# Optimization experiments

Measured on AMD Instinct MI355X. Metric: run time of the kernel, lower is better.

## Reference

```python
import jax, jax.numpy as jnp
import numpy as np

B, N, IN_F, OUT_F, H = 16, 1024, 256, 256, 4
D = OUT_F // H  # head_dim = 64
NEG_SLOPE = 0.2


def setup_inputs() -> dict:
    key = jax.random.key(0)
    k1, k2, k3 = jax.random.split(key, 3)
    h = jax.random.normal(k1, (B, N, IN_F), dtype=jnp.float32)
    mask = jnp.ones((B, N), dtype=jnp.int32)
    W = jax.random.normal(k2, (OUT_F, IN_F), dtype=jnp.float32) * (1.0 / np.sqrt(IN_F))
    a = jax.random.normal(k3, (2 * D, 1), dtype=jnp.float32) * 0.1
    return {"h": h, "mask": mask, "W": W, "a": a}


def reference(h, mask, W, a):
    # Wh = h @ W.T -> (B, N, OUT_F) -> (B, H, N, D)
    Wh = jnp.einsum('bnf,of->bno', h, W)
    Wh = Wh.reshape(h.shape[0], h.shape[1], H, D).transpose(0, 2, 1, 3)
    # Additive split: cat([Wh_i, Wh_j]) @ a == Wh_i @ a1 + Wh_j @ a2 (same math,
    # avoids the O(N^2 * 2D) concat tensor)
    a1 = a[:D, 0]  # (D,)
    a2 = a[D:, 0]  # (D,)
    s1 = jnp.einsum('bhnd,d->bhn', Wh, a1)  # score for node i
    s2 = jnp.einsum('bhnd,d->bhn', Wh, a2)  # score for node j
    e = s1[:, :, :, None] + s2[:, :, None, :]          # (B, H, N, N)
    e = jnp.where(e >= 0, e, NEG_SLOPE * e)            # LeakyReLU(0.2)
    node_mask = mask.astype(bool)                      # (B, N)
    mm = node_mask[:, None, :, None] & node_mask[:, None, None, :]  # (B,1,N,N)
    e = jnp.where(mm, e, -jnp.inf)
    attn = jax.nn.softmax(e, axis=-1)
    # dropout is identity in eval mode
    attn = jnp.where(mm, attn, 0.0)
    h_prime = jnp.einsum('bhij,bhjd->bhid', attn, Wh)  # (B, H, N, D)
    h_prime = h_prime.transpose(0, 2, 1, 3).reshape(h.shape[0], h.shape[1], OUT_F)
    return h_prime * mask.astype(h_prime.dtype)[:, :, None]
```

## Files before the change

kernel.cpp:

```cpp
#include <hip/hip_runtime.h>

typedef short short8 __attribute__((ext_vector_type(8)));
typedef float floatx4 __attribute__((ext_vector_type(4)));

#define NEG_SLOPE 0.2f

__device__ __forceinline__ unsigned short f2b(float x) {
    unsigned u = __float_as_uint(x);
    u += 0x7fffu + ((u >> 16) & 1u);
    return (unsigned short)(u >> 16);
}
__device__ __forceinline__ float b2f(unsigned short s) {
    return __uint_as_float(((unsigned)s) << 16);
}
__device__ __forceinline__ void cvt4(float4 v, ushort4& hi, ushort4& lo) {
    hi.x = f2b(v.x); hi.y = f2b(v.y); hi.z = f2b(v.z); hi.w = f2b(v.w);
    lo.x = f2b(v.x - b2f(hi.x)); lo.y = f2b(v.y - b2f(hi.y));
    lo.z = f2b(v.z - b2f(hi.z)); lo.w = f2b(v.w - b2f(hi.w));
}

__global__ __launch_bounds__(256) void k_wh(
    const float* __restrict__ hin, const int* __restrict__ mask,
    const float* __restrict__ W, const float* __restrict__ a,
    unsigned short* __restrict__ WhbT, float2* __restrict__ E1F1,
    float2* __restrict__ E2F2)
{
    __shared__ unsigned short Ahi[64 * 72], Alo[64 * 72];
    __shared__ unsigned short Bhi[128 * 72], Blo[128 * 72];

    const int t = threadIdx.x;
    const int bi = blockIdx.x;
    const int mb = bi & 15, cb = (bi >> 4) & 1, b = bi >> 5;
    const int m0 = mb * 64, n0 = cb * 128;
    const int wid = t >> 6, lane = t & 63;
    const int wm = wid >> 1, wn = wid & 1;
    const int l15 = lane & 15, q = lane >> 4;

    floatx4 acc[2][4];
#pragma unroll
    for (int mt = 0; mt < 2; ++mt)
#pragma unroll
        for (int nt = 0; nt < 4; ++nt) {
            floatx4 z = {0.f, 0.f, 0.f, 0.f};
            acc[mt][nt] = z;
        }

    for (int kt = 0; kt < 4; ++kt) {
        const int k0 = kt * 64;
#pragma unroll
        for (int p = 0; p < 4; ++p) {
            int idx = t + 256 * p;
            int row = idx >> 4, c4 = idx & 15;
            float4 v = *(const float4*)&hin[((size_t)(b * 1024 + m0 + row)) * 256 + k0 + c4 * 4];
            ushort4 hi, lo;
            cvt4(v, hi, lo);
            *(ushort4*)&Ahi[row * 72 + c4 * 4] = hi;
            *(ushort4*)&Alo[row * 72 + c4 * 4] = lo;
        }
#pragma unroll
        for (int p = 0; p < 8; ++p) {
            int idx = t + 256 * p;
            int row = idx >> 4, c4 = idx & 15;
            float4 v = *(const float4*)&W[((size_t)(n0 + row)) * 256 + k0 + c4 * 4];
            ushort4 hi, lo;
            cvt4(v, hi, lo);
            *(ushort4*)&Bhi[row * 72 + c4 * 4] = hi;
            *(ushort4*)&Blo[row * 72 + c4 * 4] = lo;
        }
        __syncthreads();
#pragma unroll
        for (int ks = 0; ks < 2; ++ks) {
            short8 ah[2], al[2], bh[4], bl[4];
#pragma unroll
            for (int mt = 0; mt < 2; ++mt) {
                int r = wm * 32 + mt * 16 + l15;
                ah[mt] = *(const short8*)&Ahi[r * 72 + ks * 32 + q * 8];
                al[mt] = *(const short8*)&Alo[r * 72 + ks * 32 + q * 8];
            }
#pragma unroll
            for (int nt = 0; nt < 4; ++nt) {
                int r = wn * 64 + nt * 16 + l15;
                bh[nt] = *(const short8*)&Bhi[r * 72 + ks * 32 + q * 8];
                bl[nt] = *(const short8*)&Blo[r * 72 + ks * 32 + q * 8];
            }
#pragma unroll
            for (int mt = 0; mt < 2; ++mt)
#pragma unroll
                for (int nt = 0; nt < 4; ++nt) {
                    acc[mt][nt] = __builtin_amdgcn_mfma_f32_16x16x32_bf16(ah[mt], bh[nt], acc[mt][nt], 0, 0, 0);
                    acc[mt][nt] = __builtin_amdgcn_mfma_f32_16x16x32_bf16(ah[mt], bl[nt], acc[mt][nt], 0, 0, 0);
                    acc[mt][nt] = __builtin_amdgcn_mfma_f32_16x16x32_bf16(al[mt], bh[nt], acc[mt][nt], 0, 0, 0);
                }
        }
        __syncthreads();
    }

    const int hh = cb * 2 + wn;
    const int b4h = b * 4 + hh;

    float a1v[4], a2v[4];
#pragma unroll
    for (int nt = 0; nt < 4; ++nt) {
        a1v[nt] = a[nt * 16 + l15];
        a2v[nt] = a[64 + nt * 16 + l15];
    }

#pragma unroll
    for (int mt = 0; mt < 2; ++mt)
#pragma unroll
        for (int nt = 0; nt < 4; ++nt) {
            int d = nt * 16 + l15;
            int i0r = m0 + wm * 32 + mt * 16 + q * 4;
            ushort4 wv;
            wv.x = f2b(acc[mt][nt][0]);
            wv.y = f2b(acc[mt][nt][1]);
            wv.z = f2b(acc[mt][nt][2]);
            wv.w = f2b(acc[mt][nt][3]);
            *(ushort4*)&WhbT[((size_t)(b4h * 64 + d)) * 1024 + i0r] = wv;
        }

    float s1p[2][4], s2p[2][4];
#pragma unroll
    for (int mt = 0; mt < 2; ++mt)
#pragma unroll
        for (int r = 0; r < 4; ++r) {
            float s1 = 0.f, s2 = 0.f;
#pragma unroll
            for (int nt = 0; nt < 4; ++nt) {
                s1 += acc[mt][nt][r] * a1v[nt];
                s2 += acc[mt][nt][r] * a2v[nt];
            }
            s1p[mt][r] = s1;
            s2p[mt][r] = s2;
        }
#pragma unroll
    for (int off = 1; off <= 8; off <<= 1)
#pragma unroll
        for (int mt = 0; mt < 2; ++mt)
#pragma unroll
            for (int r = 0; r < 4; ++r) {
                s1p[mt][r] += __shfl_xor(s1p[mt][r], off, 64);
                s2p[mt][r] += __shfl_xor(s2p[mt][r], off, 64);
            }

    if (l15 == 0) {
#pragma unroll
        for (int mt = 0; mt < 2; ++mt)
#pragma unroll
            for (int r = 0; r < 4; ++r) {
                int i = m0 + wm * 32 + mt * 16 + q * 4 + r;
                float s1 = s1p[mt][r], s2 = s2p[mt][r];
                E1F1[(size_t)b4h * 1024 + i] = make_float2(__expf(s1), __expf(NEG_SLOPE * s1));
                int mj = mask[b * 1024 + i];
                float e2 = mj ? __expf(s2) : 0.f;
                float g2 = mj ? __expf(NEG_SLOPE * s2) : 0.f;
                E2F2[(size_t)b4h * 1024 + i] = make_float2(e2, g2);
            }
    }
}

__global__ __launch_bounds__(256) void k_attn(
    const int* __restrict__ mask,
    const unsigned short* __restrict__ WhbT,
    const float2* __restrict__ E1F1, const float2* __restrict__ E2F2,
    float* __restrict__ out)
{
    __shared__ unsigned short sB[64 * 136];
    __shared__ float2 sEF[128];

    const int t = threadIdx.x;
    const int bi = blockIdx.x;
    const int ib = bi & 7, hh = (bi >> 3) & 3, b = bi >> 5;
    const int i0 = ib * 128;
    const int b4h = b * 4 + hh;
    const int wid = t >> 6, lane = t & 63;
    const int l15 = lane & 15, q = lane >> 4;
    const int iw = i0 + wid * 32;

    float E1v[2], F1v[2];
#pragma unroll
    for (int mt = 0; mt < 2; ++mt) {
        float2 e = E1F1[(size_t)b4h * 1024 + iw + mt * 16 + l15];
        E1v[mt] = e.x;
        F1v[mt] = e.y;
    }

    floatx4 acc[2][4];
#pragma unroll
    for (int mt = 0; mt < 2; ++mt)
#pragma unroll
        for (int nt = 0; nt < 4; ++nt) {
            floatx4 z = {0.f, 0.f, 0.f, 0.f};
            acc[mt][nt] = z;
        }
    float rs[2] = {0.f, 0.f};

    for (int jt = 0; jt < 8; ++jt) {
        const int j0 = jt * 128;
#pragma unroll
        for (int p = 0; p < 4; ++p) {
            int c = t + 256 * p;
            int d = c >> 4, jc = c & 15;
            *(int4*)&sB[d * 136 + jc * 8] =
                *(const int4*)&WhbT[((size_t)(b4h * 64 + d)) * 1024 + j0 + jc * 8];
        }
        if (t < 128) sEF[t] = E2F2[(size_t)b4h * 1024 + j0 + t];
        __syncthreads();

#pragma unroll
        for (int ks = 0; ks < 4; ++ks) {
            const int jl = ks * 32 + q * 8;
            float2 ef[8];
#pragma unroll
            for (int jj = 0; jj < 8; ++jj) ef[jj] = sEF[jl + jj];
            short8 bf[4];
#pragma unroll
            for (int nt = 0; nt < 4; ++nt)
                bf[nt] = *(const short8*)&sB[(nt * 16 + l15) * 136 + jl];
#pragma unroll
            for (int mt = 0; mt < 2; ++mt) {
                short8 af;
                float r0 = 0.f;
#pragma unroll
                for (int jj = 0; jj < 8; ++jj) {
                    float w = fmaxf(E1v[mt] * ef[jj].x, F1v[mt] * ef[jj].y);
                    r0 += w;
                    af[jj] = (short)f2b(w);
                }
                rs[mt] += r0;
#pragma unroll
                for (int nt = 0; nt < 4; ++nt)
                    acc[mt][nt] = __builtin_amdgcn_mfma_f32_16x16x32_bf16(af, bf[nt], acc[mt][nt], 0, 0, 0);
            }
        }
        __syncthreads();
    }

#pragma unroll
    for (int mt = 0; mt < 2; ++mt) {
        rs[mt] += __shfl_xor(rs[mt], 16, 64);
        rs[mt] += __shfl_xor(rs[mt], 32, 64);
    }

#pragma unroll
    for (int mt = 0; mt < 2; ++mt)
#pragma unroll
        for (int r = 0; r < 4; ++r) {
            int i = iw + mt * 16 + q * 4 + r;
            float l = __shfl(rs[mt], q * 4 + r, 64);
            int mi = mask[b * 1024 + i];
            float inv = (mi && l > 0.f) ? 1.0f / l : 0.f;
#pragma unroll
            for (int nt = 0; nt < 4; ++nt)
                out[((size_t)(b * 1024 + i)) * 256 + hh * 64 + nt * 16 + l15] =
                    acc[mt][nt][r] * inv;
        }
}

extern "C" void kernel_launch(void* const* d_in, const int* in_sizes, int n_in,
                              void* d_out, int out_size, void* d_ws, size_t ws_size,
                              hipStream_t stream) {
    const float* h = (const float*)d_in[0];
    const int* mask = (const int*)d_in[1];
    const float* W = (const float*)d_in[2];
    const float* a = (const float*)d_in[3];
    float* out = (float*)d_out;

    unsigned short* WhbT = (unsigned short*)d_ws;
    float2* E1F1 = (float2*)((char*)d_ws + (size_t)16 * 4 * 64 * 1024 * 2);
    float2* E2F2 = E1F1 + 16 * 4 * 1024;

    hipLaunchKernelGGL(k_wh, dim3(512), dim3(256), 0, stream, h, mask, W, a, WhbT, E1F1, E2F2);
    hipLaunchKernelGGL(k_attn, dim3(512), dim3(256), 0, stream, mask, WhbT, E1F1, E2F2, out);
}
```

Before: 108.6 us.

## Store Wh in MFMA fragment layout and double-buffer attention loads via global_load_lds

The projection kernel now writes Wh in the exact per-lane MFMA B-fragment order, and the attention kernel streams it into LDS with direct global-to-LDS loads. It double-buffers those tiles so the next tile loads while the current one computes. Both kernels use smaller tiles and twice as many blocks, with occupancy hints, and head scores are reduced across warps through shared memory. Float-to-bf16 conversion switches to byte-permute packing; the hi/lo split and the attention weights now truncate instead of rounding. This reduces LDS transpose traffic and load latency, at the cost of slightly different rounding in the weights and row sums.

```diff
diff --git a/kernel.cpp b/kernel.cpp
--- a/kernel.cpp
+++ b/kernel.cpp
@@ -2,45 +2,56 @@
 
 typedef short short8 __attribute__((ext_vector_type(8)));
 typedef float floatx4 __attribute__((ext_vector_type(4)));
+typedef unsigned int u32;
 
 #define NEG_SLOPE 0.2f
 
-__device__ __forceinline__ unsigned short f2b(float x) {
-    unsigned u = __float_as_uint(x);
-    u += 0x7fffu + ((u >> 16) & 1u);
-    return (unsigned short)(u >> 16);
-}
-__device__ __forceinline__ float b2f(unsigned short s) {
-    return __uint_as_float(((unsigned)s) << 16);
-}
-__device__ __forceinline__ void cvt4(float4 v, ushort4& hi, ushort4& lo) {
-    hi.x = f2b(v.x); hi.y = f2b(v.y); hi.z = f2b(v.z); hi.w = f2b(v.w);
-    lo.x = f2b(v.x - b2f(hi.x)); lo.y = f2b(v.y - b2f(hi.y));
-    lo.z = f2b(v.z - b2f(hi.z)); lo.w = f2b(v.w - b2f(hi.w));
-}
-
-__global__ __launch_bounds__(256) void k_wh(
+__device__ __forceinline__ u32 pk_rtne(float a, float b) {
+    u32 ua = __float_as_uint(a); ua += 0x7fffu + ((ua >> 16) & 1u);
+    u32 ub = __float_as_uint(b); ub += 0x7fffu + ((ub >> 16) & 1u);
+    return __builtin_amdgcn_perm(ub, ua, 0x07060302);
+}
+__device__ __forceinline__ u32 pk_trunc(float a, float b) {
+    return __builtin_amdgcn_perm(__float_as_uint(b), __float_as_uint(a), 0x07060302);
+}
+__device__ __forceinline__ void split_pk(float a, float b, u32& hi, u32& lo) {
+    u32 ua = __float_as_uint(a), ub = __float_as_uint(b);
+    hi = __builtin_amdgcn_perm(ub, ua, 0x07060302);
+    float la = a - __uint_as_float(ua & 0xffff0000u);
+    float lb = b - __uint_as_float(ub & 0xffff0000u);
+    lo = __builtin_amdgcn_perm(__float_as_uint(lb), __float_as_uint(la), 0x07060302);
+}
+__device__ __forceinline__ void gl_lds16(const void* g, void* l) {
+    __builtin_amdgcn_global_load_lds((__attribute__((address_space(1))) u32*)(void*)g,
+                                     (__attribute__((address_space(3))) u32*)l, 16, 0, 0);
+}
+
+__global__ __launch_bounds__(256, 4) void k_wh(
     const float* __restrict__ hin, const int* __restrict__ mask,
     const float* __restrict__ W, const float* __restrict__ a,
-    unsigned short* __restrict__ WhbT, float2* __restrict__ E1F1,
+    unsigned short* __restrict__ WhF, float2* __restrict__ E1F1,
     float2* __restrict__ E2F2)
 {
     __shared__ unsigned short Ahi[64 * 72], Alo[64 * 72];
-    __shared__ unsigned short Bhi[128 * 72], Blo[128 * 72];
+    __shared__ unsigned short Bhi[64 * 72], Blo[64 * 72];
+    __shared__ float2 sred[2][64];
 
     const int t = threadIdx.x;
     const int bi = blockIdx.x;
-    const int mb = bi & 15, cb = (bi >> 4) & 1, b = bi >> 5;
-    const int m0 = mb * 64, n0 = cb * 128;
+    const int mtile = bi >> 2, cb = bi & 3;
+    const int m0g = mtile * 64;
+    const int b = m0g >> 10;
+    const int i0 = m0g & 1023;
+    const int b4h = b * 4 + cb;
     const int wid = t >> 6, lane = t & 63;
     const int wm = wid >> 1, wn = wid & 1;
     const int l15 = lane & 15, q = lane >> 4;
 
-    floatx4 acc[2][4];
+    floatx4 acc[2][2];
 #pragma unroll
     for (int mt = 0; mt < 2; ++mt)
 #pragma unroll
-        for (int nt = 0; nt < 4; ++nt) {
+        for (int nt = 0; nt < 2; ++nt) {
             floatx4 z = {0.f, 0.f, 0.f, 0.f};
             acc[mt][nt] = z;
         }
@@ -51,26 +62,28 @@
         for (int p = 0; p < 4; ++p) {
             int idx = t + 256 * p;
             int row = idx >> 4, c4 = idx & 15;
-            float4 v = *(const float4*)&hin[((size_t)(b * 1024 + m0 + row)) * 256 + k0 + c4 * 4];
-            ushort4 hi, lo;
-            cvt4(v, hi, lo);
-            *(ushort4*)&Ahi[row * 72 + c4 * 4] = hi;
-            *(ushort4*)&Alo[row * 72 + c4 * 4] = lo;
-        }
-#pragma unroll
-        for (int p = 0; p < 8; ++p) {
+            float4 v = *(const float4*)&hin[((size_t)(m0g + row)) * 256 + k0 + c4 * 4];
+            u32 h0, l0, h1, l1;
+            split_pk(v.x, v.y, h0, l0);
+            split_pk(v.z, v.w, h1, l1);
+            *(uint2*)&Ahi[row * 72 + c4 * 4] = make_uint2(h0, h1);
+            *(uint2*)&Alo[row * 72 + c4 * 4] = make_uint2(l0, l1);
+        }
+#pragma unroll
+        for (int p = 0; p < 4; ++p) {
             int idx = t + 256 * p;
             int row = idx >> 4, c4 = idx & 15;
-            float4 v = *(const float4*)&W[((size_t)(n0 + row)) * 256 + k0 + c4 * 4];
-            ushort4 hi, lo;
-            cvt4(v, hi, lo);
-            *(ushort4*)&Bhi[row * 72 + c4 * 4] = hi;
-            *(ushort4*)&Blo[row * 72 + c4 * 4] = lo;
+            float4 v = *(const float4*)&W[((size_t)(cb * 64 + row)) * 256 + k0 + c4 * 4];
+            u32 h0, l0, h1, l1;
+            split_pk(v.x, v.y, h0, l0);
+            split_pk(v.z, v.w, h1, l1);
+            *(uint2*)&Bhi[row * 72 + c4 * 4] = make_uint2(h0, h1);
+            *(uint2*)&Blo[row * 72 + c4 * 4] = make_uint2(l0, l1);
         }
         __syncthreads();
 #pragma unroll
         for (int ks = 0; ks < 2; ++ks) {
-            short8 ah[2], al[2], bh[4], bl[4];
+            short8 ah[2], al[2], bh[2], bl[2];
 #pragma unroll
             for (int mt = 0; mt < 2; ++mt) {
                 int r = wm * 32 + mt * 16 + l15;
@@ -78,15 +91,15 @@
                 al[mt] = *(const short8*)&Alo[r * 72 + ks * 32 + q * 8];
             }
 #pragma unroll
-            for (int nt = 0; nt < 4; ++nt) {
-                int r = wn * 64 + nt * 16 + l15;
+            for (int nt = 0; nt < 2; ++nt) {
+                int r = wn * 32 + nt * 16 + l15;
                 bh[nt] = *(const short8*)&Bhi[r * 72 + ks * 32 + q * 8];
                 bl[nt] = *(const short8*)&Blo[r * 72 + ks * 32 + q * 8];
             }
 #pragma unroll
             for (int mt = 0; mt < 2; ++mt)
 #pragma unroll
-                for (int nt = 0; nt < 4; ++nt) {
+                for (int nt = 0; nt < 2; ++nt) {
                     acc[mt][nt] = __builtin_amdgcn_mfma_f32_16x16x32_bf16(ah[mt], bh[nt], acc[mt][nt], 0, 0, 0);
                     acc[mt][nt] = __builtin_amdgcn_mfma_f32_16x16x32_bf16(ah[mt], bl[nt], acc[mt][nt], 0, 0, 0);
                     acc[mt][nt] = __builtin_amdgcn_mfma_f32_16x16x32_bf16(al[mt], bh[nt], acc[mt][nt], 0, 0, 0);
@@ -95,43 +108,32 @@
         __syncthreads();
     }
 
-    const int hh = cb * 2 + wn;
-    const int b4h = b * 4 + hh;
-
-    float a1v[4], a2v[4];
-#pragma unroll
-    for (int nt = 0; nt < 4; ++nt) {
-        a1v[nt] = a[nt * 16 + l15];
-        a2v[nt] = a[64 + nt * 16 + l15];
-    }
-
+    const int c32 = (i0 + wm * 32) >> 5;
+#pragma unroll
+    for (int nt = 0; nt < 2; ++nt) {
+        int nt_a = wn * 2 + nt;
+        uint4 v;
+        v.x = pk_rtne(acc[0][nt][0], acc[0][nt][1]);
+        v.y = pk_rtne(acc[0][nt][2], acc[0][nt][3]);
+        v.z = pk_rtne(acc[1][nt][0], acc[1][nt][1]);
+        v.w = pk_rtne(acc[1][nt][2], acc[1][nt][3]);
+        *(uint4*)&WhF[(size_t)(((b4h * 32 + c32) * 4 + nt_a) * 64 + lane) * 8] = v;
+    }
+
+    float a1v[2], a2v[2];
+#pragma unroll
+    for (int nt = 0; nt < 2; ++nt) {
+        int d = wn * 32 + nt * 16 + l15;
+        a1v[nt] = a[d];
+        a2v[nt] = a[64 + d];
+    }
+    float s1p[2][4], s2p[2][4];
 #pragma unroll
     for (int mt = 0; mt < 2; ++mt)
 #pragma unroll
-        for (int nt = 0; nt < 4; ++nt) {
-            int d = nt * 16 + l15;
-            int i0r = m0 + wm * 32 + mt * 16 + q * 4;
-            ushort4 wv;
-            wv.x = f2b(acc[mt][nt][0]);
-            wv.y = f2b(acc[mt][nt][1]);
-            wv.z = f2b(acc[mt][nt][2]);
-            wv.w = f2b(acc[mt][nt][3]);
-            *(ushort4*)&WhbT[((size_t)(b4h * 64 + d)) * 1024 + i0r] = wv;
-        }
-
-    float s1p[2][4], s2p[2][4];
-#pragma unroll
-    for (int mt = 0; mt < 2; ++mt)
-#pragma unroll
         for (int r = 0; r < 4; ++r) {
-            float s1 = 0.f, s2 = 0.f;
-#pragma unroll
-            for (int nt = 0; nt < 4; ++nt) {
-                s1 += acc[mt][nt][r] * a1v[nt];
-                s2 += acc[mt][nt][r] * a2v[nt];
-            }
-            s1p[mt][r] = s1;
-            s2p[mt][r] = s2;
+            s1p[mt][r] = acc[mt][0][r] * a1v[0] + acc[mt][1][r] * a1v[1];
+            s2p[mt][r] = acc[mt][0][r] * a2v[0] + acc[mt][1][r] * a2v[1];
         }
 #pragma unroll
     for (int off = 1; off <= 8; off <<= 1)
@@ -142,119 +144,120 @@
                 s1p[mt][r] += __shfl_xor(s1p[mt][r], off, 64);
                 s2p[mt][r] += __shfl_xor(s2p[mt][r], off, 64);
             }
-
     if (l15 == 0) {
 #pragma unroll
         for (int mt = 0; mt < 2; ++mt)
 #pragma unroll
-            for (int r = 0; r < 4; ++r) {
-                int i = m0 + wm * 32 + mt * 16 + q * 4 + r;
-                float s1 = s1p[mt][r], s2 = s2p[mt][r];
-                E1F1[(size_t)b4h * 1024 + i] = make_float2(__expf(s1), __expf(NEG_SLOPE * s1));
-                int mj = mask[b * 1024 + i];
-                float e2 = mj ? __expf(s2) : 0.f;
-                float g2 = mj ? __expf(NEG_SLOPE * s2) : 0.f;
-                E2F2[(size_t)b4h * 1024 + i] = make_float2(e2, g2);
-            }
-    }
-}
-
-__global__ __launch_bounds__(256) void k_attn(
+            for (int r = 0; r < 4; ++r)
+                sred[wn][wm * 32 + mt * 16 + q * 4 + r] = make_float2(s1p[mt][r], s2p[mt][r]);
+    }
+    __syncthreads();
+    if (t < 64) {
+        float s1 = sred[0][t].x + sred[1][t].x;
+        float s2 = sred[0][t].y + sred[1][t].y;
+        int i = i0 + t;
+        E1F1[(size_t)b4h * 1024 + i] = make_float2(__expf(s1), __expf(NEG_SLOPE * s1));
+        int mj = mask[b * 1024 + i];
+        E2F2[(size_t)b4h * 1024 + i] =
+            make_float2(mj ? __expf(s2) : 0.f, mj ? __expf(NEG_SLOPE * s2) : 0.f);
+    }
+}
+
+__global__ __launch_bounds__(256, 4) void k_attn(
     const int* __restrict__ mask,
-    const unsigned short* __restrict__ WhbT,
+    const unsigned short* __restrict__ WhF,
     const float2* __restrict__ E1F1, const float2* __restrict__ E2F2,
     float* __restrict__ out)
 {
-    __shared__ unsigned short sB[64 * 136];
-    __shared__ float2 sEF[128];
+    __shared__ unsigned short sB[2][8192];
+    __shared__ float2 sEF[2][128];
 
     const int t = threadIdx.x;
     const int bi = blockIdx.x;
-    const int ib = bi & 7, hh = (bi >> 3) & 3, b = bi >> 5;
-    const int i0 = ib * 128;
+    const int ib = bi & 15, hh = (bi >> 4) & 3, b = bi >> 6;
+    const int i0 = ib * 64;
     const int b4h = b * 4 + hh;
     const int wid = t >> 6, lane = t & 63;
     const int l15 = lane & 15, q = lane >> 4;
-    const int iw = i0 + wid * 32;
-
-    float E1v[2], F1v[2];
-#pragma unroll
-    for (int mt = 0; mt < 2; ++mt) {
-        float2 e = E1F1[(size_t)b4h * 1024 + iw + mt * 16 + l15];
-        E1v[mt] = e.x;
-        F1v[mt] = e.y;
-    }
-
-    floatx4 acc[2][4];
-#pragma unroll
-    for (int mt = 0; mt < 2; ++mt)
-#pragma unroll
-        for (int nt = 0; nt < 4; ++nt) {
-            floatx4 z = {0.f, 0.f, 0.f, 0.f};
-            acc[mt][nt] = z;
-        }
-    float rs[2] = {0.f, 0.f};
+    const int iw = i0 + wid * 16;
+
+    float2 e1 = E1F1[(size_t)b4h * 1024 + iw + l15];
+    const float E1 = e1.x, F1 = e1.y;
+
+    floatx4 acc[4];
+#pragma unroll
+    for (int nt = 0; nt < 4; ++nt) {
+        floatx4 z = {0.f, 0.f, 0.f, 0.f};
+        acc[nt] = z;
+    }
+    float rs = 0.f;
+
+    const char* gbase = (const char*)WhF + (size_t)b4h * 131072;
+
+    {
+        const char* gp = gbase;
+#pragma unroll
+        for (int i = 0; i < 4; ++i)
+            gl_lds16(gp + wid * 4096 + i * 1024 + lane * 16,
+                     (char*)&sB[0][0] + wid * 4096 + i * 1024);
+        if (t < 128) sEF[0][t] = E2F2[(size_t)b4h * 1024 + t];
+    }
 
     for (int jt = 0; jt < 8; ++jt) {
-        const int j0 = jt * 128;
-#pragma unroll
-        for (int p = 0; p < 4; ++p) {
-            int c = t + 256 * p;
-            int d = c >> 4, jc = c & 15;
-            *(int4*)&sB[d * 136 + jc * 8] =
-                *(const int4*)&WhbT[((size_t)(b4h * 64 + d)) * 1024 + j0 + jc * 8];
-        }
-        if (t < 128) sEF[t] = E2F2[(size_t)b4h * 1024 + j0 + t];
+        const int buf = jt & 1;
         __syncthreads();
-
+        if (jt < 7) {
+            const char* gp = gbase + (size_t)(jt + 1) * 16384;
+#pragma unroll
+            for (int i = 0; i < 4; ++i)
+                gl_lds16(gp + wid * 4096 + i * 1024 + lane * 16,
+                         (char*)&sB[buf ^ 1][0] + wid * 4096 + i * 1024);
+            if (t < 128) sEF[buf ^ 1][t] = E2F2[(size_t)b4h * 1024 + (jt + 1) * 128 + t];
+        }
 #pragma unroll
         for (int ks = 0; ks < 4; ++ks) {
-            const int jl = ks * 32 + q * 8;
-            float2 ef[8];
-#pragma unroll
-            for (int jj = 0; jj < 8; ++jj) ef[jj] = sEF[jl + jj];
-            short8 bf[4];
-#pragma unroll
-            for (int nt = 0; nt < 4; ++nt)
-                bf[nt] = *(const short8*)&sB[(nt * 16 + l15) * 136 + jl];
-#pragma unroll
-            for (int mt = 0; mt < 2; ++mt) {
-                short8 af;
-                float r0 = 0.f;
-#pragma unroll
-                for (int jj = 0; jj < 8; ++jj) {
-                    float w = fmaxf(E1v[mt] * ef[jj].x, F1v[mt] * ef[jj].y);
-                    r0 += w;
-                    af[jj] = (short)f2b(w);
-                }
-                rs[mt] += r0;
-#pragma unroll
-                for (int nt = 0; nt < 4; ++nt)
-                    acc[mt][nt] = __builtin_amdgcn_mfma_f32_16x16x32_bf16(af, bf[nt], acc[mt][nt], 0, 0, 0);
-            }
-        }
-        __syncthreads();
-    }
-
-#pragma unroll
-    for (int mt = 0; mt < 2; ++mt) {
-        rs[mt] += __shfl_xor(rs[mt], 16, 64);
-        rs[mt] += __shfl_xor(rs[mt], 32, 64);
-    }
-
-#pragma unroll
-    for (int mt = 0; mt < 2; ++mt)
-#pragma unroll
-        for (int r = 0; r < 4; ++r) {
-            int i = iw + mt * 16 + q * 4 + r;
-            float l = __shfl(rs[mt], q * 4 + r, 64);
-            int mi = mask[b * 1024 + i];
-            float inv = (mi && l > 0.f) ? 1.0f / l : 0.f;
-#pragma unroll
-            for (int nt = 0; nt < 4; ++nt)
-                out[((size_t)(b * 1024 + i)) * 256 + hh * 64 + nt * 16 + l15] =
-                    acc[mt][nt][r] * inv;
-        }
+            const float4 eA0 = *(const float4*)&sEF[buf][ks * 32 + q * 4];
+            const float4 eA1 = *(const float4*)&sEF[buf][ks * 32 + q * 4 + 2];
+            const float4 eB0 = *(const float4*)&sEF[buf][ks * 32 + 16 + q * 4];
+            const float4 eB1 = *(const float4*)&sEF[buf][ks * 32 + 16 + q * 4 + 2];
+            float w0 = fmaxf(E1 * eA0.x, F1 * eA0.y);
+            float w1 = fmaxf(E1 * eA0.z, F1 * eA0.w);
+            float w2 = fmaxf(E1 * eA1.x, F1 * eA1.y);
+            float w3 = fmaxf(E1 * eA1.z, F1 * eA1.w);
+            float w4 = fmaxf(E1 * eB0.x, F1 * eB0.y);
+            float w5 = fmaxf(E1 * eB0.z, F1 * eB0.w);
+            float w6 = fmaxf(E1 * eB1.x, F1 * eB1.y);
+            float w7 = fmaxf(E1 * eB1.z, F1 * eB1.w);
+            union { short8 s; u32 u[4]; } af;
+            af.u[0] = pk_trunc(w0, w1);
+            af.u[1] = pk_trunc(w2, w3);
+            af.u[2] = pk_trunc(w4, w5);
+            af.u[3] = pk_trunc(w6, w7);
+#pragma unroll
+            for (int uu = 0; uu < 4; ++uu)
+                rs += __uint_as_float(af.u[uu] << 16) +
+                      __uint_as_float(af.u[uu] & 0xffff0000u);
+#pragma unroll
+            for (int nt = 0; nt < 4; ++nt) {
+                short8 bf = *(const short8*)&sB[buf][(ks * 4 + nt) * 512 + lane * 8];
+                acc[nt] = __builtin_amdgcn_mfma_f32_16x16x32_bf16(af.s, bf, acc[nt], 0, 0, 0);
+            }
+        }
+    }
+
+    rs += __shfl_xor(rs, 16, 64);
+    rs += __shfl_xor(rs, 32, 64);
+
+#pragma unroll
+    for (int r = 0; r < 4; ++r) {
+        int i = iw + q * 4 + r;
+        float l = __shfl(rs, q * 4 + r, 64);
+        int mi = mask[b * 1024 + i];
+        float inv = (mi && l > 0.f) ? 1.0f / l : 0.f;
+#pragma unroll
+        for (int nt = 0; nt < 4; ++nt)
+            out[((size_t)(b * 1024 + i)) * 256 + hh * 64 + nt * 16 + l15] = acc[nt][r] * inv;
+    }
 }
 
 extern "C" void kernel_launch(void* const* d_in, const int* in_sizes, int n_in,
@@ -266,10 +269,10 @@
     const float* a = (const float*)d_in[3];
     float* out = (float*)d_out;
 
-    unsigned short* WhbT = (unsigned short*)d_ws;
-    float2* E1F1 = (float2*)((char*)d_ws + (size_t)16 * 4 * 64 * 1024 * 2);
-    float2* E2F2 = E1F1 + 16 * 4 * 1024;
-
-    hipLaunchKernelGGL(k_wh, dim3(512), dim3(256), 0, stream, h, mask, W, a, WhbT, E1F1, E2F2);
-    hipLaunchKernelGGL(k_attn, dim3(512), dim3(256), 0, stream, mask, WhbT, E1F1, E2F2, out);
-}
+    unsigned short* WhF = (unsigned short*)d_ws;
+    float2* E1F1 = (float2*)((char*)d_ws + (size_t)64 * 32 * 4 * 64 * 8 * 2);
+    float2* E2F2 = E1F1 + 64 * 1024;
+
+    hipLaunchKernelGGL(k_wh, dim3(1024), dim3(256), 0, stream, h, mask, W, a, WhF, E1F1, E2F2);
+    hipLaunchKernelGGL(k_attn, dim3(1024), dim3(256), 0, stream, mask, WhF, E1F1, E2F2, out);
+}
```

Result: no change. 109.2 us (+0.6%).
